# Optimization experiments

Hardware: AMD Instinct MI355X
Metric: run time of the kernel (lower is better)

Reference implementation:

```python
import jax, jax.numpy as jnp
import numpy as np

MAX_FREQ = 3
OMEGA = 0.5 * np.pi
SQRT2 = float(np.sqrt(2.0))


def _embed(x, max_freq, omega):
    # x: (Q,) -> (Q, 2*max_freq+1) : [1, sqrt2*cos(1*w*x), sqrt2*sin(1*w*x), ...]
    freqs = jnp.arange(1, max_freq + 1, dtype=x.dtype) * jnp.asarray(omega, x.dtype)
    ang = x[:, None] * freqs  # (Q, n)
    cs = jnp.stack([jnp.cos(ang), jnp.sin(ang)], axis=-1).reshape(x.shape[0], 2 * max_freq)
    return jnp.concatenate([jnp.ones((x.shape[0], 1), x.dtype), SQRT2 * cs], axis=-1)


def setup_inputs() -> dict:
    key = jax.random.key(0)
    feat = jax.random.normal(key, (4, 147, 64, 64), dtype=jnp.float32)
    return {"feat": feat, "h": 256, "w": 256, "flip1": 1, "flip3": 2}


def reference(feat, h, w, flip1, flip3):
    N, C3, H, W = feat.shape
    c = C3 // 3  # (2*max_freq+1)^2
    n1 = 2 * MAX_FREQ + 1
    dt = feat.dtype
    Q = h * w

    # make_coord((h, w)): centers of grid cells in [-1, 1]; channel0 over h-axis
    xs = (-1.0 + (2.0 * jnp.arange(h, dtype=dt) + 1.0) / h)
    ys = (-1.0 + (2.0 * jnp.arange(w, dtype=dt) + 1.0) / w)
    cx, cy = jnp.meshgrid(xs, ys, indexing='ij')
    coord = jnp.stack([cx.ravel(), cy.ravel()], axis=-1)  # (Q, 2)
    if flip1 == 1:
        coord = coord * jnp.array([1.0, -1.0], dtype=dt)
    elif flip1 == 2:
        coord = coord * jnp.array([-1.0, 1.0], dtype=dt)
    elif flip1 == 4:
        coord = -coord

    rx = 1.0 / H  # 2 / H / 2
    ry = 1.0 / W
    eps_shift = 1e-06

    feat_flat = jnp.transpose(feat, (0, 2, 3, 1)).reshape(N, H * W, C3)  # (N, H*W, C3)

    preds = []
    areas = []
    for vx in (-1, 1):
        for vy in (-1, 1):
            shift = jnp.array([vx * rx + eps_shift, vy * ry + eps_shift], dtype=dt)
            coord_ = jnp.clip(coord + shift, -1.0 + 1e-06, 1.0 - 1e-06)  # (Q, 2)
            # grid_sample nearest, align_corners=False: unnormalize then round-half-even
            ih = jnp.clip(jnp.round(((coord_[:, 0] + 1.0) * H - 1.0) * 0.5).astype(jnp.int32), 0, H - 1)
            iw = jnp.clip(jnp.round(((coord_[:, 1] + 1.0) * W - 1.0) * 0.5).astype(jnp.int32), 0, W - 1)
            latent = jnp.take(feat_flat, ih * W + iw, axis=1)  # (N, Q, 3c)
            # q_coord equals cell-center coords at the gathered index
            qh = -1.0 + (2.0 * ih.astype(dt) + 1.0) / H
            qw = -1.0 + (2.0 * iw.astype(dt) + 1.0) / W
            rel0 = (coord[:, 0] - qh) * H  # (Q,)
            rel1 = (coord[:, 1] - qw) * W
            if flip3 == 1:
                rel1 = -rel1
            elif flip3 == 2:
                rel0 = -rel0
            elif flip3 == 4:
                rel0, rel1 = -rel0, -rel1
            ex = _embed(rel0, MAX_FREQ, OMEGA)  # (Q, n1)
            ey = _embed(rel1, MAX_FREQ, OMEGA)
            ope = (ex[:, :, None] * ey[:, None, :]).reshape(Q, c)  # (Q, c)
            pred = jnp.einsum('qc,nqkc->nqk', ope, latent.reshape(N, Q, 3, c))  # (N, Q, 3)
            preds.append(pred)
            areas.append(jnp.abs(rel0 * rel1) + 1e-09)

    tot_area = areas[0] + areas[1] + areas[2] + areas[3]  # (Q,)
    areas = [areas[3], areas[2], areas[1], areas[0]]  # diagonal swap
    ret = preds[0] * (areas[0] / tot_area)[None, :, None]
    for p, a in zip(preds[1:], areas[1:]):
        ret = ret + p * (a / tot_area)[None, :, None]
    return jnp.transpose(ret.reshape(N, h, w, 3), (0, 3, 1, 2))
```

## Files before the change

kernel.cpp:

```cpp
#include <hip/hip_runtime.h>
#include <math.h>


#define FH 64
#define FW 64
#define FHW 4096
#define NC3 147
#define OHW 256

__device__ __forceinline__ void embed7(float r, float e[7]) {
    const float F1  = 1.5707963705062866f;
    const float SQ2 = 1.4142135381698608f;
    float a = r * F1;
    float s1 = __sinf(a), c1 = __cosf(a);
    float s2 = 2.0f * s1 * c1, c2 = c1 * c1 - s1 * s1;
    float s3 = s2 * c1 + c2 * s1, c3 = c2 * c1 - s2 * s1;
    e[0] = 1.0f;
    e[1] = SQ2 * c1; e[2] = SQ2 * s1;
    e[3] = SQ2 * c2; e[4] = SQ2 * s2;
    e[5] = SQ2 * c3; e[6] = SQ2 * s3;
}

__global__ __launch_bounds__(256, 3) void ope_render_kernel(
    const float* __restrict__ feat,
    const int* __restrict__ pflip1,
    const int* __restrict__ pflip3,
    float* __restrict__ out)
{
    const int tid = threadIdx.x;
    const int k   = blockIdx.x;
    const int ib  = blockIdx.y;
    const int n   = blockIdx.z;
    const int flip1 = pflip1[0];
    const int flip3 = pflip3[0];

    const bool boundary = (ib == 0);
    const int rA = boundary ? 0  : (ib - 1);
    const int rB = boundary ? 63 : ib;

    const int m  = tid >> 6;
    const int jg = tid & 63;
    const bool fx = (flip1 == 2) || (flip1 == 4);
    const bool fy = (flip1 == 1) || (flip1 == 4);
    const bool o  = (jg == 0);
    const float sgx = (flip3 == 2 || flip3 == 4) ? -1.0f : 1.0f;
    const float sgy = (flip3 == 1 || flip3 == 4) ? -1.0f : 1.0f;

    const int i_e = boundary ? ((m < 2) ? m : 252 + m) : (4 * ib - 2 + m);
    const float cx = -1.0f + (2.0f * (float)i_e + 1.0f) * (1.0f / 256.0f);
    const int row0 = boundary ? ((m >> 1) ? rB : rA) : rA;
    const float qh0 = -1.0f + (2.0f * (float)row0 + 1.0f) * (1.0f / 64.0f);
    const float rel0_0 = (cx - qh0) * 64.0f;
    const float rel0_1 = boundary ? rel0_0 : (rel0_0 - 2.0f);

    float ex0[7], ex1[7];
    embed7(sgx * rel0_0, ex0);
    {
        const float xm = boundary ? 1.0f : -1.0f;
        ex1[0] = 1.0f;
        ex1[1] = xm * ex0[1]; ex1[2] = xm * ex0[2];
        ex1[3] = ex0[3];      ex1[4] = ex0[4];
        ex1[5] = xm * ex0[5]; ex1[6] = xm * ex0[6];
    }

    const float* __restrict__ b0 =
        feat + (((size_t)n * NC3 + k * 49) * FH + row0) * FW + jg;
    float cv0[7], cv1[7];
    #pragma unroll
    for (int b = 0; b < 7; ++b) { cv0[b] = 0.0f; cv1[b] = 0.0f; }
    if (!boundary) {
        const float* __restrict__ b1 = b0 + (rB - rA) * FW;
        #pragma unroll
        for (int c = 0; c < 49; ++c) {
            cv0[c % 7] = fmaf(ex0[c / 7], b0[c * FHW], cv0[c % 7]);
            cv1[c % 7] = fmaf(ex1[c / 7], b1[c * FHW], cv1[c % 7]);
        }
    } else {
        #pragma unroll
        for (int c = 0; c < 49; ++c)
            cv0[c % 7] = fmaf(ex0[c / 7], b0[c * FHW], cv0[c % 7]);
        #pragma unroll
        for (int b = 0; b < 7; ++b) cv1[b] = cv0[b];
    }

    const int srcl = (jg + 63) & 63;
    float qv0[7], qv1[7];
    #pragma unroll
    for (int b = 0; b < 7; ++b) {
        qv0[b] = __shfl(cv0[b], srcl, 64);
        qv1[b] = __shfl(cv1[b], srcl, 64);
    }

    const float tm = o ? 0.0f : -2.0f;
    const float ym = o ? 1.0f : -1.0f;
    float acc0, acc1, acc2, acc3;
    #pragma unroll
    for (int p = 0; p < 2; ++p) {
        const int jb = o ? (p ? 254 : 0) : (4 * jg - 2 + 2 * p);
        const int cm = o ? (p ? 63 : 0) : (jg - 1);
        const float qwm = -1.0f + (2.0f * (float)cm + 1.0f) * (1.0f / 64.0f);

        float A0[7], A1[7], B0[7], B1[7];
        #pragma unroll
        for (int b = 0; b < 7; ++b) {
            if (p == 0) {
                A0[b] = o ? cv0[b] : qv0[b];
                A1[b] = o ? cv1[b] : qv1[b];
                B0[b] = cv0[b];
                B1[b] = cv1[b];
            } else {
                A0[b] = qv0[b];
                A1[b] = qv1[b];
                B0[b] = o ? qv0[b] : cv0[b];
                B1[b] = o ? qv1[b] : cv1[b];
            }
        }
        #pragma unroll
        for (int sub = 0; sub < 2; ++sub) {
            const int j_e = jb + sub;
            const float cy = -1.0f + (2.0f * (float)j_e + 1.0f) * (1.0f / 256.0f);
            const float rel1m = (cy - qwm) * 64.0f;
            const float rel1p = rel1m + tm;

            float a00 = fabsf(rel0_0 * rel1m) + 1e-9f;
            float a01 = fabsf(rel0_0 * rel1p) + 1e-9f;
            float a10 = fabsf(rel0_1 * rel1m) + 1e-9f;
            float a11 = fabsf(rel0_1 * rel1p) + 1e-9f;
            float tot = ((a00 + a01) + a10) + a11;
            float rinv = __builtin_amdgcn_rcpf(tot);
            const float w00 = a11 * rinv, w01 = a10 * rinv;
            const float w10 = a01 * rinv, w11 = a00 * rinv;

            float ey0[7], ey1[7];
            embed7(sgy * rel1m, ey0);
            ey1[0] = 1.0f;
            ey1[1] = ym * ey0[1]; ey1[2] = ym * ey0[2];
            ey1[3] = ey0[3];      ey1[4] = ey0[4];
            ey1[5] = ym * ey0[5]; ey1[6] = ym * ey0[6];

            float v00 = 0.0f, v01 = 0.0f, v10 = 0.0f, v11 = 0.0f;
            #pragma unroll
            for (int b = 0; b < 7; ++b) {
                v00 = fmaf(A0[b], ey0[b], v00);
                v10 = fmaf(A1[b], ey0[b], v10);
                v01 = fmaf(B0[b], ey1[b], v01);
                v11 = fmaf(B1[b], ey1[b], v11);
            }
            float r = fmaf(v00, w00, fmaf(v01, w01, fmaf(v10, w10, v11 * w11)));
            if (p == 0) { if (sub == 0) acc0 = r; else acc1 = r; }
            else        { if (sub == 0) acc2 = r; else acc3 = r; }
        }
    }

    const int i_out = fx ? (255 - i_e) : i_e;
    float* __restrict__ ob = out + (((size_t)n * 3 + k) * OHW + i_out) * OHW;
    const int jA = o ? 0   : (4 * jg - 2);
    const int jB = o ? 254 : (4 * jg);
    if (!fy) {
        *(float2*)&ob[jA] = make_float2(acc0, acc1);
        *(float2*)&ob[jB] = make_float2(acc2, acc3);
    } else {
        *(float2*)&ob[254 - jA] = make_float2(acc1, acc0);
        *(float2*)&ob[254 - jB] = make_float2(acc3, acc2);
    }
}

extern "C" void kernel_launch(void* const* d_in, const int* in_sizes, int n_in,
                              void* d_out, int out_size, void* d_ws, size_t ws_size,
                              hipStream_t stream) {
    const float* feat  = (const float*)d_in[0];
    const int*   flip1 = (const int*)d_in[3];
    const int*   flip3 = (const int*)d_in[4];
    float*       out   = (float*)d_out;

    dim3 grid(3, 64, 4);
    dim3 block(256);
    hipLaunchKernelGGL(ope_render_kernel, grid, block, 0, stream,
                       feat, flip1, flip3, out);
}
```

Measured before the change: 10.84 us.

## Split channel loads across lane pairs with float2 reads and xor-shuffle reduce

Each pair of adjacent lanes now shares two feature columns. One lane handles channel rows 0-3 and the other rows 4-6, each loading float2 vectors instead of scalars. The partial column sums are then exchanged with a shfl_xor to rebuild each lane's own column contraction. This roughly halves the global load instructions per thread, at the cost of extra shuffles, padded redundant loads for the odd lane, and more select logic.

```diff
diff --git a/kernel.cpp b/kernel.cpp
--- a/kernel.cpp
+++ b/kernel.cpp
@@ -40,6 +40,8 @@
 
     const int m  = tid >> 6;
     const int jg = tid & 63;
+    const int par  = jg & 1;
+    const int colp = jg & ~1;
     const bool fx = (flip1 == 2) || (flip1 == 4);
     const bool fy = (flip1 == 1) || (flip1 == 4);
     const bool o  = (jg == 0);
@@ -63,22 +65,60 @@
         ex1[5] = xm * ex0[5]; ex1[6] = xm * ex0[6];
     }
 
-    const float* __restrict__ b0 =
-        feat + (((size_t)n * NC3 + k * 49) * FH + row0) * FW + jg;
+    float ex0P[4], ex1P[4];
+    #pragma unroll
+    for (int i = 0; i < 4; ++i) {
+        ex0P[i] = par ? ((i < 3) ? ex0[i + 4] : 0.0f) : ex0[i];
+        ex1P[i] = par ? ((i < 3) ? ex1[i + 4] : 0.0f) : ex1[i];
+    }
+
+    const size_t chb = (size_t)n * NC3 + k * 49 + 28 * par;
+    const float* __restrict__ p0 =
+        feat + (chb * FH + row0) * FW + colp;
+    float2 acc0[7], acc1[7];
+    #pragma unroll
+    for (int b = 0; b < 7; ++b) {
+        acc0[b] = make_float2(0.0f, 0.0f);
+        acc1[b] = make_float2(0.0f, 0.0f);
+    }
+    if (!boundary) {
+        const float* __restrict__ p1 = p0 + (rB - rA) * FW;
+        #pragma unroll
+        for (int t = 0; t < 28; ++t) {
+            const int ce = (t > 20) ? (par ? 20 : t) : t;
+            float2 v0 = *(const float2*)(p0 + (size_t)ce * FHW);
+            float2 v1 = *(const float2*)(p1 + (size_t)ce * FHW);
+            const float e0 = ex0P[t / 7];
+            const float e1 = ex1P[t / 7];
+            acc0[t % 7].x = fmaf(e0, v0.x, acc0[t % 7].x);
+            acc0[t % 7].y = fmaf(e0, v0.y, acc0[t % 7].y);
+            acc1[t % 7].x = fmaf(e1, v1.x, acc1[t % 7].x);
+            acc1[t % 7].y = fmaf(e1, v1.y, acc1[t % 7].y);
+        }
+    } else {
+        #pragma unroll
+        for (int t = 0; t < 28; ++t) {
+            const int ce = (t > 20) ? (par ? 20 : t) : t;
+            float2 v0 = *(const float2*)(p0 + (size_t)ce * FHW);
+            const float e0 = ex0P[t / 7];
+            acc0[t % 7].x = fmaf(e0, v0.x, acc0[t % 7].x);
+            acc0[t % 7].y = fmaf(e0, v0.y, acc0[t % 7].y);
+        }
+    }
+
     float cv0[7], cv1[7];
     #pragma unroll
-    for (int b = 0; b < 7; ++b) { cv0[b] = 0.0f; cv1[b] = 0.0f; }
-    if (!boundary) {
-        const float* __restrict__ b1 = b0 + (rB - rA) * FW;
-        #pragma unroll
-        for (int c = 0; c < 49; ++c) {
-            cv0[c % 7] = fmaf(ex0[c / 7], b0[c * FHW], cv0[c % 7]);
-            cv1[c % 7] = fmaf(ex1[c / 7], b1[c * FHW], cv1[c % 7]);
-        }
-    } else {
-        #pragma unroll
-        for (int c = 0; c < 49; ++c)
-            cv0[c % 7] = fmaf(ex0[c / 7], b0[c * FHW], cv0[c % 7]);
+    for (int b = 0; b < 7; ++b) {
+        float s0 = par ? acc0[b].x : acc0[b].y;
+        float o0 = par ? acc0[b].y : acc0[b].x;
+        cv0[b] = o0 + __shfl_xor(s0, 1, 64);
+        if (!boundary) {
+            float s1 = par ? acc1[b].x : acc1[b].y;
+            float o1 = par ? acc1[b].y : acc1[b].x;
+            cv1[b] = o1 + __shfl_xor(s1, 1, 64);
+        }
+    }
+    if (boundary) {
         #pragma unroll
         for (int b = 0; b < 7; ++b) cv1[b] = cv0[b];
     }
@@ -93,7 +133,7 @@
 
     const float tm = o ? 0.0f : -2.0f;
     const float ym = o ? 1.0f : -1.0f;
-    float acc0, acc1, acc2, acc3;
+    float acc_0, acc_1, acc_2, acc_3;
     #pragma unroll
     for (int p = 0; p < 2; ++p) {
         const int jb = o ? (p ? 254 : 0) : (4 * jg - 2 + 2 * p);
@@ -147,8 +187,8 @@
                 v11 = fmaf(B1[b], ey1[b], v11);
             }
             float r = fmaf(v00, w00, fmaf(v01, w01, fmaf(v10, w10, v11 * w11)));
-            if (p == 0) { if (sub == 0) acc0 = r; else acc1 = r; }
-            else        { if (sub == 0) acc2 = r; else acc3 = r; }
+            if (p == 0) { if (sub == 0) acc_0 = r; else acc_1 = r; }
+            else        { if (sub == 0) acc_2 = r; else acc_3 = r; }
         }
     }
 
@@ -157,11 +197,11 @@
     const int jA = o ? 0   : (4 * jg - 2);
     const int jB = o ? 254 : (4 * jg);
     if (!fy) {
-        *(float2*)&ob[jA] = make_float2(acc0, acc1);
-        *(float2*)&ob[jB] = make_float2(acc2, acc3);
+        *(float2*)&ob[jA] = make_float2(acc_0, acc_1);
+        *(float2*)&ob[jB] = make_float2(acc_2, acc_3);
     } else {
-        *(float2*)&ob[254 - jA] = make_float2(acc1, acc0);
-        *(float2*)&ob[254 - jB] = make_float2(acc3, acc2);
+        *(float2*)&ob[254 - jA] = make_float2(acc_1, acc_0);
+        *(float2*)&ob[254 - jB] = make_float2(acc_3, acc_2);
     }
 }
 
```

New measurement: 17.18 us. +58.5%, slower.
